# Kernel tuning notes

Hardware: AMD Instinct MI355X
Metric: run time of the kernel (lower is better)

Reference implementation:

```python
import jax, jax.numpy as jnp
from jax import lax
import numpy as np

H = 256        # hidden_dim
PRED_LEN = 96  # pred_len
B, L = 256, 512


def _gru_step(h, xt, W_ih, W_hh, b_ih, b_hh):
    # PyTorch GRU gate math. xt: [B, in], h: [B, H], W_ih: [3H, in], W_hh: [3H, H]
    gi = xt @ W_ih.T + b_ih            # [B, 3H]
    gh = h @ W_hh.T + b_hh             # [B, 3H]
    i_r, i_z, i_n = jnp.split(gi, 3, axis=-1)
    h_r, h_z, h_n = jnp.split(gh, 3, axis=-1)
    r = jax.nn.sigmoid(i_r + h_r)
    z = jax.nn.sigmoid(i_z + h_z)
    n = jnp.tanh(i_n + r * h_n)
    return (1.0 - z) * n + z * h


def _run_gru_layer(xs, W_ih, W_hh, b_ih, b_hh):
    # xs: [L, B, in] -> (ys [L, B, H], h_last [B, H])
    h0 = jnp.zeros((xs.shape[1], H), xs.dtype)
    def step(h, xt):
        hn = _gru_step(h, xt, W_ih, W_hh, b_ih, b_hh)
        return hn, hn
    h_last, ys = lax.scan(step, h0, xs)
    return ys, h_last


def setup_inputs() -> dict:
    key = jax.random.key(0)
    ks = jax.random.split(key, 16)
    s = 1.0 / np.sqrt(H)
    u = lambda k, shape: jax.random.uniform(k, shape, jnp.float32, -s, s)
    return {
        "x": jax.random.normal(ks[0], (B, 1, L), jnp.float32),
        # encoder GRU layer 0 (input_size=1)
        "W_ih0": u(ks[1], (3 * H, 1)), "W_hh0": u(ks[2], (3 * H, H)),
        "b_ih0": u(ks[3], (3 * H,)), "b_hh0": u(ks[4], (3 * H,)),
        # encoder GRU layer 1 (input_size=H)
        "W_ih1": u(ks[5], (3 * H, H)), "W_hh1": u(ks[6], (3 * H, H)),
        "b_ih1": u(ks[7], (3 * H,)), "b_hh1": u(ks[8], (3 * H,)),
        # decoder GRUCell (input_size=1)
        "Wd_ih": u(ks[9], (3 * H, 1)), "Wd_hh": u(ks[10], (3 * H, H)),
        "bd_ih": u(ks[11], (3 * H,)), "bd_hh": u(ks[12], (3 * H,)),
        # output Linear(H, 1)
        "Wo": u(ks[13], (1, H)), "bo": u(ks[14], (1,)),
    }


def reference(x, W_ih0, W_hh0, b_ih0, b_hh0, W_ih1, W_hh1, b_ih1, b_hh1,
              Wd_ih, Wd_hh, bd_ih, bd_hh, Wo, bo):
    # seq = x[:, 0, :].unsqueeze(-1) -> [B, L, 1]; scan wants [L, B, 1]
    xs = jnp.transpose(x[:, 0, :, None], (1, 0, 2))
    ys0, _ = _run_gru_layer(xs, W_ih0, W_hh0, b_ih0, b_hh0)
    _, h_t = _run_gru_layer(ys0, W_ih1, W_hh1, b_ih1, b_hh1)  # h_n[-1]: [B, H]
    # (dropout between layers is inactive in eval mode)

    dec_in0 = jnp.zeros((x.shape[0], 1), x.dtype)

    def dec_step(carry, _):
        h, inp = carry
        h = _gru_step(h, inp, Wd_ih, Wd_hh, bd_ih, bd_hh)
        step = h @ Wo.T + bo           # [B, 1]
        return (h, step), step

    _, steps = lax.scan(dec_step, (h_t, dec_in0), None, length=PRED_LEN)
    # steps: [pred_len, B, 1] -> cat along dim 1 -> [B, pred_len]
    return jnp.transpose(steps[..., 0], (1, 0))
```

## Files before the change

kernel.cpp:

```cpp
#include <hip/hip_runtime.h>
#include <hip/hip_fp16.h>

#define HDIM 256
#define LSEQ 512
#define PRED 96
#define NTHR 256

typedef _Float16 f16x8 __attribute__((ext_vector_type(8)));
typedef _Float16 f16x4 __attribute__((ext_vector_type(4)));
typedef float f32x4 __attribute__((ext_vector_type(4)));
typedef unsigned int u32;

__device__ __forceinline__ float sigm(float x) { return 1.f / (1.f + __expf(-x)); }
__device__ __forceinline__ float tanh_(float x) { float t = __expf(2.f * x); return 1.f - 2.f / (t + 1.f); }
__device__ __forceinline__ float dppx1(float v) {
  return __builtin_bit_cast(float, __builtin_amdgcn_update_dpp(
      0, __builtin_bit_cast(int, v), 0xB1, 0xF, 0xF, true));
}

struct __align__(16) Smem {
  _Float16 h[2][2][256];
  _Float16 A11[4][5120];
  float tw[3][256], tb[3][256], bnh[256], wo[256];
  float xv[LSEQ];
  float red[2][4];
};

#define CAST_A(DST, SRC) asm("" : "=a"(DST) : "0"(SRC))

#define DECL_MM                                                                \
  f16x8 Aa[6][8];                                                \
  f16x8 Av[5][8];                                                \
  f32x4 ac[12];                                      \
  f32x4 zc;                                          \
  { f32x4 z4 = {0.f, 0.f, 0.f, 0.f}; asm("" : "=a"(zc) : "0"(z4)); }

#define LOADA(WPTR)                                                            \
  _Pragma("unroll") for (int tt = 0; tt < 12; ++tt) {                          \
    _Pragma("unroll") for (int kt = 0; kt < 8; ++kt) {                         \
      const float* ap = (WPTR) +                                               \
          (size_t)(256 * (tt >> 2) + 64 * w + 16 * (tt & 3) + n) * HDIM +      \
          32 * kt + 8 * q;                                                     \
      const float4 a0 = *(const float4*)ap;                                    \
      const float4 a1 = *(const float4*)(ap + 4);                              \
      f16x8 tf;                                                                \
      tf[0] = (_Float16)a0.x; tf[1] = (_Float16)a0.y;                          \
      tf[2] = (_Float16)a0.z; tf[3] = (_Float16)a0.w;                          \
      tf[4] = (_Float16)a1.x; tf[5] = (_Float16)a1.y;                          \
      tf[6] = (_Float16)a1.z; tf[7] = (_Float16)a1.w;                          \
      if (tt < 6) { CAST_A(Aa[tt][kt], tf); }                                  \
      else if (tt < 11) { Av[tt - 6][kt] = tf; }                               \
      else { *(f16x8*)(a11p + kt * 1280) = tf; }                               \
    }                                                                          \
  }

#define MM_A_S(I, AF, B) asm("v_mfma_f32_16x16x32_f16 %0, %1, %2, %3" : "=a"(ac[I]) : "a"(AF), "v"(B), "a"(zc));
#define MM_A(I, AF, B)   asm("v_mfma_f32_16x16x32_f16 %0, %1, %2, %0" : "+a"(ac[I]) : "a"(AF), "v"(B));
#define MM_V_S(I, AF, B) asm("v_mfma_f32_16x16x32_f16 %0, %1, %2, %3" : "=a"(ac[I]) : "v"(AF), "v"(B), "a"(zc));
#define MM_V(I, AF, B)   asm("v_mfma_f32_16x16x32_f16 %0, %1, %2, %0" : "+a"(ac[I]) : "v"(AF), "v"(B));

#define R12S(KT, B, AL)                                                        \
  MM_A_S(0, Aa[0][KT], B) MM_A_S(1, Aa[1][KT], B) MM_A_S(2, Aa[2][KT], B)      \
  MM_A_S(3, Aa[3][KT], B) MM_A_S(4, Aa[4][KT], B) MM_A_S(5, Aa[5][KT], B)      \
  MM_V_S(6, Av[0][KT], B) MM_V_S(7, Av[1][KT], B) MM_V_S(8, Av[2][KT], B)      \
  MM_V_S(9, Av[3][KT], B) MM_V_S(10, Av[4][KT], B) MM_V_S(11, AL, B)
#define R12(KT, B, AL)                                                         \
  MM_A(0, Aa[0][KT], B) MM_A(1, Aa[1][KT], B) MM_A(2, Aa[2][KT], B)            \
  MM_A(3, Aa[3][KT], B) MM_A(4, Aa[4][KT], B) MM_A(5, Aa[5][KT], B)            \
  MM_V(6, Av[0][KT], B) MM_V(7, Av[1][KT], B) MM_V(8, Av[2][KT], B)            \
  MM_V(9, Av[3][KT], B) MM_V(10, Av[4][KT], B) MM_V(11, AL, B)

#define MAT_STEP(PB)                                                           \
  {                                                                            \
    const char* hp = hq + (PB) * 1024;                                         \
    f16x8 b0 = *(const f16x8*)(hp);                                            \
    f16x8 b1 = *(const f16x8*)(hp + 64);                                       \
    f16x8 b2 = *(const f16x8*)(hp + 128);                                      \
    f16x8 b3 = *(const f16x8*)(hp + 192);                                      \
    f16x8 a0 = *(const f16x8*)(a11p);                                          \
    f16x8 a1 = *(const f16x8*)(a11p + 1280);                                   \
    f16x8 a2 = *(const f16x8*)(a11p + 2560);                                   \
    f16x8 a3 = *(const f16x8*)(a11p + 3840);                                   \
    R12S(0, b0, a0)                                                            \
    b0 = *(const f16x8*)(hp + 256); a0 = *(const f16x8*)(a11p + 5120);         \
    R12(1, b1, a1)                                                             \
    b1 = *(const f16x8*)(hp + 320); a1 = *(const f16x8*)(a11p + 6400);         \
    R12(2, b2, a2)                                                             \
    b2 = *(const f16x8*)(hp + 384); a2 = *(const f16x8*)(a11p + 7680);         \
    R12(3, b3, a3)                                                             \
    b3 = *(const f16x8*)(hp + 448); a3 = *(const f16x8*)(a11p + 8960);         \
    R12(4, b0, a0)                                                             \
    R12(5, b1, a1)                                                             \
    R12(6, b2, a2)                                                             \
    R12(7, b3, a3)                                                             \
  }

#define ACFENCE                                                                \
  asm volatile("s_nop 7\n\ts_nop 7"                                            \
               : "+a"(ac[0]), "+a"(ac[1]), "+a"(ac[2]), "+a"(ac[3]),           \
                 "+a"(ac[4]), "+a"(ac[5]), "+a"(ac[6]), "+a"(ac[7]),           \
                 "+a"(ac[8]), "+a"(ac[9]), "+a"(ac[10]), "+a"(ac[11]));

#define BAR asm volatile("s_waitcnt lgkmcnt(0)\n\ts_barrier" ::: "memory")

#define SELG(P, G)                                                             \
  f32x4 P;                                                                     \
  { const f32x4 e0 = ac[4 * (G)], e1 = ac[4 * (G) + 1];                        \
    const f32x4 e2 = ac[4 * (G) + 2], e3 = ac[4 * (G) + 3];                    \
    const f32x4 t0 = s1 ? e1 : e0;                                             \
    const f32x4 t1 = s1 ? e3 : e2;                                             \
    P = s2 ? t1 : t0; }
#define PSUM(P)                                                                \
  { P[0] += dppx1(P[0]); P[1] += dppx1(P[1]);                                  \
    P[2] += dppx1(P[2]); P[3] += dppx1(P[3]); }

#define GATES(GR, GZ, GN, RHOOK, STEXTRA)                                      \
  {                                                                            \
    const char* rh = hrow + pb * 1024;                                         \
    char* wh = hrow + (pb ^ 1) * 1024;                                         \
    const f16x4 hh = *(const f16x4*)(rh);                                      \
    const f16x4 hl = *(const f16x4*)(rh + 512);                                \
    const f32x4 bn4 = *(const f32x4*)bnrow;                                    \
    f16x4 vh, vl;                                                              \
    _Pragma("unroll") for (int r = 0; r < 4; ++r) {                            \
      const float rr = sigm((GR)[r] + pr[r]);                                  \
      const float zz = sigm((GZ)[r] + pz[r]);                                  \
      const float nn = tanh_(fmaf(rr, pn[r] + bn4[r], (GN)[r]));               \
      const float ho = (float)hh[r] + (float)hl[r];                            \
      const float hv = fmaf(zz, ho - nn, nn);                                  \
      vh[r] = (_Float16)hv;                                                    \
      vl[r] = (_Float16)(hv - (float)vh[r]);                                   \
      RHOOK                                                                    \
    }                                                                          \
    if (st) {                                                                  \
      *(f16x4*)(wh) = vh;                                                      \
      *(f16x4*)(wh + 512) = vl;                                                \
      STEXTRA                                                                  \
    }                                                                          \
  }

#define LANE_GEOM                                                              \
  const int tid = threadIdx.x;                                                 \
  const int w = tid >> 6, lane = tid & 63, n = lane & 15, q = lane >> 4;       \
  const int b = blockIdx.x;                                                    \
  const int sg = (n >> 1) & 3;                                                 \
  const bool s1 = (n & 2) != 0, s2 = (n & 4) != 0;                             \
  const bool st = (n == 2 * sg);     \
  const int row = 64 * w + 16 * sg + 4 * q;                                    \
  char* a11p = (char*)sm.A11 + w * 10240 + n * 80 + q * 16;                    \
  const char* hq = (const char*)sm.h + (n & 1) * 512 + q * 16;                 \
  char* hrow = (char*)sm.h + row * 2;                                          \
  const char* bnrow = (const char*)sm.bnh + row * 4;

__global__ __launch_bounds__(NTHR, 1) void gru_l0(
    const float* __restrict__ x, const float* __restrict__ Wih0,
    const float* __restrict__ Whh0, const float* __restrict__ bih0,
    const float* __restrict__ bhh0, __half* __restrict__ ys) {
  __shared__ Smem sm;
  LANE_GEOM
  DECL_MM
  const float* twrow = (const float*)sm.tw + row;
  const float* tbrow = (const float*)sm.tb + row;

  for (int e = tid; e < LSEQ; e += NTHR) sm.xv[e] = x[(size_t)b * LSEQ + e];
#pragma unroll
  for (int g = 0; g < 3; ++g) {
    sm.tw[g][tid] = Wih0[256 * g + tid];
    sm.tb[g][tid] = bih0[256 * g + tid] + (g < 2 ? bhh0[256 * g + tid] : 0.f);
  }
  sm.bnh[tid] = bhh0[512 + tid];
  ((u32*)sm.h)[tid] = 0;
  LOADA(Whh0);
  __syncthreads();

  __half* ysp = ys + (size_t)b * LSEQ * HDIM + row;
  int pb = 0;
#pragma unroll 1
  for (int t = 0; t < LSEQ; ++t) {
    const float xt = sm.xv[t];
    MAT_STEP(pb)
    ACFENCE
    SELG(pr, 0) SELG(pz, 1) SELG(pn, 2)
    PSUM(pr) PSUM(pz) PSUM(pn)
    const f32x4 gr = *(const f32x4*)(twrow) * xt + *(const f32x4*)(tbrow);
    const f32x4 gz = *(const f32x4*)(twrow + 256) * xt + *(const f32x4*)(tbrow + 256);
    const f32x4 gn = *(const f32x4*)(twrow + 512) * xt + *(const f32x4*)(tbrow + 512);
    GATES(gr, gz, gn, ;, *(f16x4*)ysp = vh;)
    ysp += HDIM;
    pb ^= 1;
    BAR;
  }
}

__global__ __launch_bounds__(256) void gemm_gi(
    const float* __restrict__ Wih1, const float* __restrict__ bih1,
    const float* __restrict__ bhh1, const __half* __restrict__ ys,
    __half* __restrict__ gi) {
  const int lane = threadIdx.x & 63;
  const int wv = threadIdx.x >> 6;
  const size_t bt0 = (size_t)blockIdx.x << 4;
  const int n = lane & 15, q = lane >> 4;

  f16x8 bfr[8];
  const __half* yrow = ys + (bt0 + n) * HDIM + q * 8;
#pragma unroll
  for (int kk = 0; kk < 8; ++kk) bfr[kk] = *(const f16x8*)(yrow + kk * 32);

#pragma unroll 1
  for (int mt = 0; mt < 12; ++mt) {
    const int j0 = (wv * 12 + mt) << 4;
    const float* arow = Wih1 + (size_t)(j0 + n) * HDIM + q * 8;
    f32x4 acc = {0.f, 0.f, 0.f, 0.f};
#pragma unroll
    for (int kk = 0; kk < 8; ++kk) {
      const float4 a0 = *(const float4*)(arow + kk * 32);
      const float4 a1 = *(const float4*)(arow + kk * 32 + 4);
      f16x8 af;
      af[0] = (_Float16)a0.x; af[1] = (_Float16)a0.y;
      af[2] = (_Float16)a0.z; af[3] = (_Float16)a0.w;
      af[4] = (_Float16)a1.x; af[5] = (_Float16)a1.y;
      af[6] = (_Float16)a1.z; af[7] = (_Float16)a1.w;
      acc = __builtin_amdgcn_mfma_f32_16x16x32_f16(af, bfr[kk], acc, 0, 0, 0);
    }
    const int jr = j0 + (q << 2);
    __half o4[4];
#pragma unroll
    for (int r2 = 0; r2 < 4; ++r2) {
      const float bb = bih1[jr + r2] + (j0 < 512 ? bhh1[jr + r2] : 0.f);
      o4[r2] = __float2half(acc[r2] + bb);
    }
    *(uint2*)(gi + (bt0 + n) * 768 + jr) = *(uint2*)o4;
  }
}

#define LOADGI(PF, T)                                                          \
  { const __half* gp = gi + ((size_t)b * LSEQ + (T)) * 768 + row;              \
    PF[0] = *(const uint2*)(gp);                                               \
    PF[1] = *(const uint2*)(gp + 256);                                         \
    PF[2] = *(const uint2*)(gp + 512); }

#define STEP3(PF)                                                              \
  {                                                                            \
    MAT_STEP(pb)                                                               \
    ACFENCE                                                                    \
    SELG(pr, 0) SELG(pz, 1) SELG(pn, 2)                                        \
    PSUM(pr) PSUM(pz) PSUM(pn)                                                 \
    const __half2* p0 = (const __half2*)&PF[0];                                \
    const __half2* p1 = (const __half2*)&PF[1];                                \
    const __half2* p2 = (const __half2*)&PF[2];                                \
    const float2 r01 = __half22float2(p0[0]), r23 = __half22float2(p0[1]);     \
    const float2 z01 = __half22float2(p1[0]), z23 = __half22float2(p1[1]);     \
    const float2 n01 = __half22float2(p2[0]), n23 = __half22float2(p2[1]);     \
    const f32x4 gr = {r01.x, r01.y, r23.x, r23.y};                             \
    const f32x4 gz = {z01.x, z01.y, z23.x, z23.y};                             \
    const f32x4 gn = {n01.x, n01.y, n23.x, n23.y};                             \
    GATES(gr, gz, gn, ;, ;)                                                    \
    pb ^= 1;                                                                   \
    BAR;                                                                       \
  }

__global__ __launch_bounds__(NTHR, 1) void gru_l1dec(
    const float* __restrict__ Whh1, const float* __restrict__ bhh1,
    const float* __restrict__ Wdih, const float* __restrict__ Wdhh,
    const float* __restrict__ bdih, const float* __restrict__ bdhh,
    const float* __restrict__ Wo, const float* __restrict__ bo,
    const __half* __restrict__ gi, float* __restrict__ outp) {
  __shared__ Smem sm;
  LANE_GEOM
  DECL_MM
  const float* twrow = (const float*)sm.tw + row;
  const float* tbrow = (const float*)sm.tb + row;
  const float* worow = (const float*)sm.wo + row;

  sm.bnh[tid] = bhh1[512 + tid];
  ((u32*)sm.h)[tid] = 0;
  LOADA(Whh1);
  __syncthreads();

  uint2 pfA[3], pfB[3];
  LOADGI(pfA, 0);
  int pb = 0;
#pragma unroll 1
  for (int t = 0; t < LSEQ; t += 2) {
    LOADGI(pfB, t + 1);
    STEP3(pfA)
    LOADGI(pfA, (t + 2 < LSEQ) ? (t + 2) : (LSEQ - 1));
    STEP3(pfB)
  }

  LOADA(Wdhh);
#pragma unroll
  for (int g = 0; g < 3; ++g) {
    sm.tw[g][tid] = Wdih[256 * g + tid];
    sm.tb[g][tid] = bdih[256 * g + tid] + (g < 2 ? bdhh[256 * g + tid] : 0.f);
  }
  sm.bnh[tid] = bdhh[512 + tid];
  sm.wo[tid] = Wo[tid];
  const float bov = bo[0];
  if (tid < 4) sm.red[0][tid] = (tid == 0) ? -bov : 0.f;
  __syncthreads();

  int rb = 0;
#pragma unroll 1
  for (int t = 0; t < PRED; ++t) {
    const f32x4 rd = *(const f32x4*)sm.red[rb];
    const float it = bov + rd[0] + rd[1] + rd[2] + rd[3];
    if (tid == 0 && t > 0) outp[(size_t)b * PRED + t - 1] = it;
    MAT_STEP(pb)
    ACFENCE
    SELG(pr, 0) SELG(pz, 1) SELG(pn, 2)
    PSUM(pr) PSUM(pz) PSUM(pn)
    const f32x4 gr = *(const f32x4*)(twrow) * it + *(const f32x4*)(tbrow);
    const f32x4 gz = *(const f32x4*)(twrow + 256) * it + *(const f32x4*)(tbrow + 256);
    const f32x4 gn = *(const f32x4*)(twrow + 512) * it + *(const f32x4*)(tbrow + 512);
    const f32x4 wo4 = *(const f32x4*)worow;
    float c = 0.f;
    GATES(gr, gz, gn, c = fmaf(wo4[r], hv, c);, ;)
    if (!st) c = 0.f;
    c += __shfl_xor(c, 2);
    c += __shfl_xor(c, 4);
    c += __shfl_xor(c, 16);
    c += __shfl_xor(c, 32);
    if (lane == 0) sm.red[rb ^ 1][w] = c;
    pb ^= 1;
    rb ^= 1;
    BAR;
  }
  if (tid == 0) {
    const f32x4 rd = *(const f32x4*)sm.red[rb];
    outp[(size_t)b * PRED + PRED - 1] = bov + rd[0] + rd[1] + rd[2] + rd[3];
  }
}

extern "C" void kernel_launch(void* const* d_in, const int* in_sizes, int n_in,
                              void* d_out, int out_size, void* d_ws, size_t ws_size,
                              hipStream_t stream) {
  const float* x    = (const float*)d_in[0];
  const float* Wih0 = (const float*)d_in[1];
  const float* Whh0 = (const float*)d_in[2];
  const float* bih0 = (const float*)d_in[3];
  const float* bhh0 = (const float*)d_in[4];
  const float* Wih1 = (const float*)d_in[5];
  const float* Whh1 = (const float*)d_in[6];
  const float* bih1 = (const float*)d_in[7];
  const float* bhh1 = (const float*)d_in[8];
  const float* Wdih = (const float*)d_in[9];
  const float* Wdhh = (const float*)d_in[10];
  const float* bdih = (const float*)d_in[11];
  const float* bdhh = (const float*)d_in[12];
  const float* Wo   = (const float*)d_in[13];
  const float* bo   = (const float*)d_in[14];

  __half* ys = (__half*)d_ws;
  __half* gi = ys + (size_t)256 * 512 * 256;

  gru_l0<<<256, NTHR, 0, stream>>>(x, Wih0, Whh0, bih0, bhh0, ys);
  gemm_gi<<<(256 * 512) / 16, 256, 0, stream>>>(Wih1, bih1, bhh1, ys, gi);
  gru_l1dec<<<256, NTHR, 0, stream>>>(Whh1, bhh1, Wdih, Wdhh, bdih, bdhh,
                                      Wo, bo, gi, (float*)d_out);
}
```

Baseline: 2.651 ms.

## Stream pre-packed fp16 recurrent weights from global with 8 waves per block

Adds a prep kernel that converts the three recurrent weight matrices to fp16 once and stores them in an MFMA-fragment-friendly layout in a global buffer. The recurrent kernels now use 512 threads (8 waves) and reload half of the weight fragments from global/L2 every timestep while issuing MFMAs, instead of keeping all weights in registers plus LDS. This frees register and LDS pressure and spreads the per-step matmul across twice as many waves, at the cost of per-step global weight traffic and an extra launch.

```diff
diff --git a/kernel.cpp b/kernel.cpp
--- a/kernel.cpp
+++ b/kernel.cpp
@@ -4,12 +4,14 @@
 #define HDIM 256
 #define LSEQ 512
 #define PRED 96
-#define NTHR 256
+#define NTHR 512
 
 typedef _Float16 f16x8 __attribute__((ext_vector_type(8)));
 typedef _Float16 f16x4 __attribute__((ext_vector_type(4)));
 typedef float f32x4 __attribute__((ext_vector_type(4)));
 typedef unsigned int u32;
+
+__device__ __align__(16) _Float16 wpk_g[3 * 196608];
 
 __device__ __forceinline__ float sigm(float x) { return 1.f / (1.f + __expf(-x)); }
 __device__ __forceinline__ float tanh_(float x) { float t = __expf(2.f * x); return 1.f - 2.f / (t + 1.f); }
@@ -20,105 +22,72 @@
 
 struct __align__(16) Smem {
   _Float16 h[2][2][256];
-  _Float16 A11[4][5120];
   float tw[3][256], tb[3][256], bnh[256], wo[256];
   float xv[LSEQ];
-  float red[2][4];
+  float red[2][8];
 };
 
-#define CAST_A(DST, SRC) asm("" : "=a"(DST) : "0"(SRC))
-
-#define DECL_MM                                                                \
-  f16x8 Aa[6][8];                                                \
-  f16x8 Av[5][8];                                                \
-  f32x4 ac[12];                                      \
-  f32x4 zc;                                          \
-  { f32x4 z4 = {0.f, 0.f, 0.f, 0.f}; asm("" : "=a"(zc) : "0"(z4)); }
-
-#define LOADA(WPTR)                                                            \
-  _Pragma("unroll") for (int tt = 0; tt < 12; ++tt) {                          \
-    _Pragma("unroll") for (int kt = 0; kt < 8; ++kt) {                         \
-      const float* ap = (WPTR) +                                               \
-          (size_t)(256 * (tt >> 2) + 64 * w + 16 * (tt & 3) + n) * HDIM +      \
-          32 * kt + 8 * q;                                                     \
-      const float4 a0 = *(const float4*)ap;                                    \
-      const float4 a1 = *(const float4*)(ap + 4);                              \
-      f16x8 tf;                                                                \
-      tf[0] = (_Float16)a0.x; tf[1] = (_Float16)a0.y;                          \
-      tf[2] = (_Float16)a0.z; tf[3] = (_Float16)a0.w;                          \
-      tf[4] = (_Float16)a1.x; tf[5] = (_Float16)a1.y;                          \
-      tf[6] = (_Float16)a1.z; tf[7] = (_Float16)a1.w;                          \
-      if (tt < 6) { CAST_A(Aa[tt][kt], tf); }                                  \
-      else if (tt < 11) { Av[tt - 6][kt] = tf; }                               \
-      else { *(f16x8*)(a11p + kt * 1280) = tf; }                               \
-    }                                                                          \
-  }
-
-#define MM_A_S(I, AF, B) asm("v_mfma_f32_16x16x32_f16 %0, %1, %2, %3" : "=a"(ac[I]) : "a"(AF), "v"(B), "a"(zc));
-#define MM_A(I, AF, B)   asm("v_mfma_f32_16x16x32_f16 %0, %1, %2, %0" : "+a"(ac[I]) : "a"(AF), "v"(B));
-#define MM_V_S(I, AF, B) asm("v_mfma_f32_16x16x32_f16 %0, %1, %2, %3" : "=a"(ac[I]) : "v"(AF), "v"(B), "a"(zc));
-#define MM_V(I, AF, B)   asm("v_mfma_f32_16x16x32_f16 %0, %1, %2, %0" : "+a"(ac[I]) : "v"(AF), "v"(B));
-
-#define R12S(KT, B, AL)                                                        \
-  MM_A_S(0, Aa[0][KT], B) MM_A_S(1, Aa[1][KT], B) MM_A_S(2, Aa[2][KT], B)      \
-  MM_A_S(3, Aa[3][KT], B) MM_A_S(4, Aa[4][KT], B) MM_A_S(5, Aa[5][KT], B)      \
-  MM_V_S(6, Av[0][KT], B) MM_V_S(7, Av[1][KT], B) MM_V_S(8, Av[2][KT], B)      \
-  MM_V_S(9, Av[3][KT], B) MM_V_S(10, Av[4][KT], B) MM_V_S(11, AL, B)
-#define R12(KT, B, AL)                                                         \
-  MM_A(0, Aa[0][KT], B) MM_A(1, Aa[1][KT], B) MM_A(2, Aa[2][KT], B)            \
-  MM_A(3, Aa[3][KT], B) MM_A(4, Aa[4][KT], B) MM_A(5, Aa[5][KT], B)            \
-  MM_V(6, Av[0][KT], B) MM_V(7, Av[1][KT], B) MM_V(8, Av[2][KT], B)            \
-  MM_V(9, Av[3][KT], B) MM_V(10, Av[4][KT], B) MM_V(11, AL, B)
-
-#define MAT_STEP(PB)                                                           \
-  {                                                                            \
-    const char* hp = hq + (PB) * 1024;                                         \
-    f16x8 b0 = *(const f16x8*)(hp);                                            \
-    f16x8 b1 = *(const f16x8*)(hp + 64);                                       \
-    f16x8 b2 = *(const f16x8*)(hp + 128);                                      \
-    f16x8 b3 = *(const f16x8*)(hp + 192);                                      \
-    f16x8 a0 = *(const f16x8*)(a11p);                                          \
-    f16x8 a1 = *(const f16x8*)(a11p + 1280);                                   \
-    f16x8 a2 = *(const f16x8*)(a11p + 2560);                                   \
-    f16x8 a3 = *(const f16x8*)(a11p + 3840);                                   \
-    R12S(0, b0, a0)                                                            \
-    b0 = *(const f16x8*)(hp + 256); a0 = *(const f16x8*)(a11p + 5120);         \
-    R12(1, b1, a1)                                                             \
-    b1 = *(const f16x8*)(hp + 320); a1 = *(const f16x8*)(a11p + 6400);         \
-    R12(2, b2, a2)                                                             \
-    b2 = *(const f16x8*)(hp + 384); a2 = *(const f16x8*)(a11p + 7680);         \
-    R12(3, b3, a3)                                                             \
-    b3 = *(const f16x8*)(hp + 448); a3 = *(const f16x8*)(a11p + 8960);         \
-    R12(4, b0, a0)                                                             \
-    R12(5, b1, a1)                                                             \
-    R12(6, b2, a2)                                                             \
-    R12(7, b3, a3)                                                             \
-  }
-
-#define ACFENCE                                                                \
-  asm volatile("s_nop 7\n\ts_nop 7"                                            \
-               : "+a"(ac[0]), "+a"(ac[1]), "+a"(ac[2]), "+a"(ac[3]),           \
-                 "+a"(ac[4]), "+a"(ac[5]), "+a"(ac[6]), "+a"(ac[7]),           \
-                 "+a"(ac[8]), "+a"(ac[9]), "+a"(ac[10]), "+a"(ac[11]));
-
-#define BAR asm volatile("s_waitcnt lgkmcnt(0)\n\ts_barrier" ::: "memory")
-
-#define SELG(P, G)                                                             \
-  f32x4 P;                                                                     \
-  { const f32x4 e0 = ac[4 * (G)], e1 = ac[4 * (G) + 1];                        \
-    const f32x4 e2 = ac[4 * (G) + 2], e3 = ac[4 * (G) + 3];                    \
-    const f32x4 t0 = s1 ? e1 : e0;                                             \
-    const f32x4 t1 = s1 ? e3 : e2;                                             \
-    P = s2 ? t1 : t0; }
+#define DECL8                                                                  \
+  f32x4 ac[6];                 \
+  f32x4 zc;                                                                    \
+  { f32x4 z4 = {0.f, 0.f, 0.f, 0.f}; asm("" : "=a"(zc) : "0"(z4)); }           \
+  f16x8 wA[6], wB[6], wC[6], wD[6];
+
+#define LOADW(DST, KT)                                                         \
+  { _Pragma("unroll") for (int tau = 0; tau < 6; ++tau)                        \
+      DST[tau] = *(const f16x8*)(wbase + ((KT) * 6 + tau) * 512 + lane * 8); }
+
+#define MMW_S(I, AF, B) asm volatile("v_mfma_f32_16x16x32_f16 %0, %1, %2, %3" : "=a"(ac[I]) : "v"(AF), "v"(B), "a"(zc));
+#define MMW(I, AF, B)   asm volatile("v_mfma_f32_16x16x32_f16 %0, %1, %2, %0" : "+a"(ac[I]) : "v"(AF), "v"(B));
+#define MM6_S(WF, B) MMW_S(0, WF[0], B) MMW_S(1, WF[1], B) MMW_S(2, WF[2], B)  \
+                     MMW_S(3, WF[3], B) MMW_S(4, WF[4], B) MMW_S(5, WF[5], B)
+#define MM6(WF, B)   MMW(0, WF[0], B) MMW(1, WF[1], B) MMW(2, WF[2], B)        \
+                     MMW(3, WF[3], B) MMW(4, WF[4], B) MMW(5, WF[5], B)
+
+#define VMW0 asm volatile("s_waitcnt vmcnt(0)" ::: "memory");
+
+#define FENCE                                                                  \
+  asm volatile("s_nop 7\n\ts_nop 7\n\ts_nop 7\n\ts_nop 7\n\t"                  \
+               "s_nop 7\n\ts_nop 7\n\ts_nop 7\n\ts_nop 7"                      \
+               : "+a"(ac[0]), "+a"(ac[1]), "+a"(ac[2]),                        \
+                 "+a"(ac[3]), "+a"(ac[4]), "+a"(ac[5]));                       \
+  __builtin_amdgcn_sched_barrier(0);
+
+#define BAR asm volatile("s_waitcnt vmcnt(0) lgkmcnt(0)\n\ts_barrier" ::: "memory")
+
+#define SELG2(P, G)                                                            \
+  { const f32x4 e0 = ac[2 * (G)], e1 = ac[2 * (G) + 1]; P = s1 ? e1 : e0; }
 #define PSUM(P)                                                                \
   { P[0] += dppx1(P[0]); P[1] += dppx1(P[1]);                                  \
     P[2] += dppx1(P[2]); P[3] += dppx1(P[3]); }
 
-#define GATES(GR, GZ, GN, RHOOK, STEXTRA)                                      \
+#define LDH(OFF) (*(const f16x8*)(hp + (OFF)))
+
+#define MCORE8(PB, ...)                                                        \
+  {                                                                            \
+    const char* hp = hq + (PB) * 1024;                                         \
+    f16x8 u0 = LDH(0), u1 = LDH(64), u2 = LDH(128), u3 = LDH(192);             \
+    __VA_ARGS__                                                                \
+    MM6_S(wA, u0) u0 = LDH(256); LOADW(wA, 4)                                  \
+    MM6(wB, u1)   u1 = LDH(320); LOADW(wB, 5)                                  \
+    MM6(wC, u2)   u2 = LDH(384); LOADW(wC, 6)                                  \
+    MM6(wD, u3)   u3 = LDH(448); LOADW(wD, 7)                                  \
+    VMW0                                                                       \
+    MM6(wA, u0)   LOADW(wA, 0)                                                 \
+    MM6(wB, u1)   LOADW(wB, 1)                                                 \
+    MM6(wC, u2)   LOADW(wC, 2)                                                 \
+    MM6(wD, u3)   LOADW(wD, 3)                                                 \
+    FENCE                                                                      \
+    SELG2(pr, 0) PSUM(pr)                                                      \
+    SELG2(pz, 1) PSUM(pz)                                                      \
+    SELG2(pn, 2) PSUM(pn)                                                      \
+  }
+
+#define GTAIL8(GR, GZ, GN, RHOOK, STEXTRA)                                     \
   {                                                                            \
     const char* rh = hrow + pb * 1024;                                         \
     char* wh = hrow + (pb ^ 1) * 1024;                                         \
-    const f16x4 hh = *(const f16x4*)(rh);                                      \
+    const f16x4 hh = *(const f16x4*)rh;                                        \
     const f16x4 hl = *(const f16x4*)(rh + 512);                                \
     const f32x4 bn4 = *(const f32x4*)bnrow;                                    \
     f16x4 vh, vl;                                                              \
@@ -133,44 +102,71 @@
       RHOOK                                                                    \
     }                                                                          \
     if (st) {                                                                  \
-      *(f16x4*)(wh) = vh;                                                      \
+      *(f16x4*)wh = vh;                                                        \
       *(f16x4*)(wh + 512) = vl;                                                \
       STEXTRA                                                                  \
     }                                                                          \
   }
 
-#define LANE_GEOM                                                              \
+#define LANE_GEOM8                                                             \
   const int tid = threadIdx.x;                                                 \
   const int w = tid >> 6, lane = tid & 63, n = lane & 15, q = lane >> 4;       \
   const int b = blockIdx.x;                                                    \
-  const int sg = (n >> 1) & 3;                                                 \
-  const bool s1 = (n & 2) != 0, s2 = (n & 4) != 0;                             \
-  const bool st = (n == 2 * sg);     \
-  const int row = 64 * w + 16 * sg + 4 * q;                                    \
-  char* a11p = (char*)sm.A11 + w * 10240 + n * 80 + q * 16;                    \
+  const bool s1 = (n & 2) != 0;                                                \
+  const bool st = (n & 13) == 0;      \
+  const int sg1 = (n >> 1) & 1;                                                \
+  const int row = 32 * w + 16 * sg1 + 4 * q;                                   \
   const char* hq = (const char*)sm.h + (n & 1) * 512 + q * 16;                 \
   char* hrow = (char*)sm.h + row * 2;                                          \
   const char* bnrow = (const char*)sm.bnh + row * 4;
 
-__global__ __launch_bounds__(NTHR, 1) void gru_l0(
-    const float* __restrict__ x, const float* __restrict__ Wih0,
-    const float* __restrict__ Whh0, const float* __restrict__ bih0,
-    const float* __restrict__ bhh0, __half* __restrict__ ys) {
+__global__ __launch_bounds__(256) void prep(const float* __restrict__ W0,
+                                            const float* __restrict__ W1,
+                                            const float* __restrict__ Wd) {
+  const int idx = blockIdx.x * 256 + threadIdx.x;
+  const int lane = idx & 63;
+  int t2 = idx >> 6;
+  const int tau = t2 % 6; t2 /= 6;
+  const int kt = t2 & 7;  t2 >>= 3;
+  const int w = t2 & 7;   t2 >>= 3;
+  const int L = t2;
+  const float* W = (L == 0) ? W0 : ((L == 1) ? W1 : Wd);
+  const int g = tau >> 1, s = tau & 1, n = lane & 15, q = lane >> 4;
+  const int r = 256 * g + 32 * w + 16 * s + n;
+  const int c = 32 * kt + 8 * q;
+  const float4 a0 = *(const float4*)(W + (size_t)r * HDIM + c);
+  const float4 a1 = *(const float4*)(W + (size_t)r * HDIM + c + 4);
+  f16x8 tf;
+  tf[0] = (_Float16)a0.x; tf[1] = (_Float16)a0.y;
+  tf[2] = (_Float16)a0.z; tf[3] = (_Float16)a0.w;
+  tf[4] = (_Float16)a1.x; tf[5] = (_Float16)a1.y;
+  tf[6] = (_Float16)a1.z; tf[7] = (_Float16)a1.w;
+  *(f16x8*)(wpk_g + (size_t)L * 196608 + (size_t)w * 24576 +
+            (kt * 6 + tau) * 512 + lane * 8) = tf;
+}
+
+__global__ __attribute__((amdgpu_flat_work_group_size(NTHR, NTHR), amdgpu_waves_per_eu(2)))
+void gru_l0(const float* __restrict__ x, const float* __restrict__ Wih0,
+            const float* __restrict__ bih0, const float* __restrict__ bhh0,
+            __half* __restrict__ ys) {
   __shared__ Smem sm;
-  LANE_GEOM
-  DECL_MM
-  const float* twrow = (const float*)sm.tw + row;
-  const float* tbrow = (const float*)sm.tb + row;
-
-  for (int e = tid; e < LSEQ; e += NTHR) sm.xv[e] = x[(size_t)b * LSEQ + e];
-#pragma unroll
-  for (int g = 0; g < 3; ++g) {
-    sm.tw[g][tid] = Wih0[256 * g + tid];
-    sm.tb[g][tid] = bih0[256 * g + tid] + (g < 2 ? bhh0[256 * g + tid] : 0.f);
-  }
-  sm.bnh[tid] = bhh0[512 + tid];
+  LANE_GEOM8
+  DECL8
+  const _Float16* wbase = wpk_g + (size_t)w * 24576;
+  const char* twp = (const char*)sm.tw + row * 4;
+  const char* tbp = (const char*)sm.tb + row * 4;
+
+  sm.xv[tid] = x[(size_t)b * LSEQ + tid];
+  if (tid < 256) {
+#pragma unroll
+    for (int g = 0; g < 3; ++g) {
+      sm.tw[g][tid] = Wih0[256 * g + tid];
+      sm.tb[g][tid] = bih0[256 * g + tid] + (g < 2 ? bhh0[256 * g + tid] : 0.f);
+    }
+    sm.bnh[tid] = bhh0[512 + tid];
+  }
   ((u32*)sm.h)[tid] = 0;
-  LOADA(Whh0);
+  LOADW(wA, 0) LOADW(wB, 1) LOADW(wC, 2) LOADW(wD, 3)
   __syncthreads();
 
   __half* ysp = ys + (size_t)b * LSEQ * HDIM + row;
@@ -178,14 +174,12 @@
 #pragma unroll 1
   for (int t = 0; t < LSEQ; ++t) {
     const float xt = sm.xv[t];
-    MAT_STEP(pb)
-    ACFENCE
-    SELG(pr, 0) SELG(pz, 1) SELG(pn, 2)
-    PSUM(pr) PSUM(pz) PSUM(pn)
-    const f32x4 gr = *(const f32x4*)(twrow) * xt + *(const f32x4*)(tbrow);
-    const f32x4 gz = *(const f32x4*)(twrow + 256) * xt + *(const f32x4*)(tbrow + 256);
-    const f32x4 gn = *(const f32x4*)(twrow + 512) * xt + *(const f32x4*)(tbrow + 512);
-    GATES(gr, gz, gn, ;, *(f16x4*)ysp = vh;)
+    f32x4 pr, pz, pn;
+    MCORE8(pb, ;)
+    const f32x4 g_r = *(const f32x4*)twp * xt + *(const f32x4*)tbp;
+    const f32x4 g_z = *(const f32x4*)(twp + 1024) * xt + *(const f32x4*)(tbp + 1024);
+    const f32x4 g_n = *(const f32x4*)(twp + 2048) * xt + *(const f32x4*)(tbp + 2048);
+    GTAIL8(g_r, g_z, g_n, ;, *(f16x4*)ysp = vh;)
     ysp += HDIM;
     pb ^= 1;
     BAR;
@@ -239,86 +233,77 @@
     PF[1] = *(const uint2*)(gp + 256);                                         \
     PF[2] = *(const uint2*)(gp + 512); }
 
-#define STEP3(PF)                                                              \
-  {                                                                            \
-    MAT_STEP(pb)                                                               \
-    ACFENCE                                                                    \
-    SELG(pr, 0) SELG(pz, 1) SELG(pn, 2)                                        \
-    PSUM(pr) PSUM(pz) PSUM(pn)                                                 \
-    const __half2* p0 = (const __half2*)&PF[0];                                \
-    const __half2* p1 = (const __half2*)&PF[1];                                \
-    const __half2* p2 = (const __half2*)&PF[2];                                \
-    const float2 r01 = __half22float2(p0[0]), r23 = __half22float2(p0[1]);     \
-    const float2 z01 = __half22float2(p1[0]), z23 = __half22float2(p1[1]);     \
-    const float2 n01 = __half22float2(p2[0]), n23 = __half22float2(p2[1]);     \
-    const f32x4 gr = {r01.x, r01.y, r23.x, r23.y};                             \
-    const f32x4 gz = {z01.x, z01.y, z23.x, z23.y};                             \
-    const f32x4 gn = {n01.x, n01.y, n23.x, n23.y};                             \
-    GATES(gr, gz, gn, ;, ;)                                                    \
-    pb ^= 1;                                                                   \
-    BAR;                                                                       \
-  }
-
-__global__ __launch_bounds__(NTHR, 1) void gru_l1dec(
-    const float* __restrict__ Whh1, const float* __restrict__ bhh1,
-    const float* __restrict__ Wdih, const float* __restrict__ Wdhh,
-    const float* __restrict__ bdih, const float* __restrict__ bdhh,
-    const float* __restrict__ Wo, const float* __restrict__ bo,
-    const __half* __restrict__ gi, float* __restrict__ outp) {
+__global__ __attribute__((amdgpu_flat_work_group_size(NTHR, NTHR), amdgpu_waves_per_eu(2)))
+void gru_l1dec(const float* __restrict__ bhh1, const float* __restrict__ Wdih,
+               const float* __restrict__ bdih, const float* __restrict__ bdhh,
+               const float* __restrict__ Wo, const float* __restrict__ bo,
+               const __half* __restrict__ gi, float* __restrict__ outp) {
   __shared__ Smem sm;
-  LANE_GEOM
-  DECL_MM
-  const float* twrow = (const float*)sm.tw + row;
-  const float* tbrow = (const float*)sm.tb + row;
-  const float* worow = (const float*)sm.wo + row;
-
-  sm.bnh[tid] = bhh1[512 + tid];
+  LANE_GEOM8
+  DECL8
+  const _Float16* wbase = wpk_g + 196608 + (size_t)w * 24576;
+  const char* twp = (const char*)sm.tw + row * 4;
+  const char* tbp = (const char*)sm.tb + row * 4;
+  const char* wop = (const char*)sm.wo + row * 4;
+
+  if (tid < 256) sm.bnh[tid] = bhh1[512 + tid];
   ((u32*)sm.h)[tid] = 0;
-  LOADA(Whh1);
+  LOADW(wA, 0) LOADW(wB, 1) LOADW(wC, 2) LOADW(wD, 3)
   __syncthreads();
 
-  uint2 pfA[3], pfB[3];
-  LOADGI(pfA, 0);
   int pb = 0;
 #pragma unroll 1
-  for (int t = 0; t < LSEQ; t += 2) {
-    LOADGI(pfB, t + 1);
-    STEP3(pfA)
-    LOADGI(pfA, (t + 2 < LSEQ) ? (t + 2) : (LSEQ - 1));
-    STEP3(pfB)
-  }
-
-  LOADA(Wdhh);
-#pragma unroll
-  for (int g = 0; g < 3; ++g) {
-    sm.tw[g][tid] = Wdih[256 * g + tid];
-    sm.tb[g][tid] = bdih[256 * g + tid] + (g < 2 ? bdhh[256 * g + tid] : 0.f);
-  }
-  sm.bnh[tid] = bdhh[512 + tid];
-  sm.wo[tid] = Wo[tid];
+  for (int t = 0; t < LSEQ; ++t) {
+    uint2 pf[3];
+    f32x4 pr, pz, pn;
+    MCORE8(pb, LOADGI(pf, t))
+    const __half2* p0 = (const __half2*)&pf[0];
+    const __half2* p1 = (const __half2*)&pf[1];
+    const __half2* p2 = (const __half2*)&pf[2];
+    const float2 r01 = __half22float2(p0[0]), r23 = __half22float2(p0[1]);
+    const float2 z01 = __half22float2(p1[0]), z23 = __half22float2(p1[1]);
+    const float2 n01 = __half22float2(p2[0]), n23 = __half22float2(p2[1]);
+    const f32x4 g_r = {r01.x, r01.y, r23.x, r23.y};
+    const f32x4 g_z = {z01.x, z01.y, z23.x, z23.y};
+    const f32x4 g_n = {n01.x, n01.y, n23.x, n23.y};
+    GTAIL8(g_r, g_z, g_n, ;, ;)
+    pb ^= 1;
+    BAR;
+  }
+
+  wbase = wpk_g + 2 * 196608 + (size_t)w * 24576;
+  if (tid < 256) {
+#pragma unroll
+    for (int g = 0; g < 3; ++g) {
+      sm.tw[g][tid] = Wdih[256 * g + tid];
+      sm.tb[g][tid] = bdih[256 * g + tid] + (g < 2 ? bdhh[256 * g + tid] : 0.f);
+    }
+    sm.bnh[tid] = bdhh[512 + tid];
+    sm.wo[tid] = Wo[tid];
+  }
   const float bov = bo[0];
-  if (tid < 4) sm.red[0][tid] = (tid == 0) ? -bov : 0.f;
+  if (tid < 8) sm.red[0][tid] = (tid == 0) ? -bov : 0.f;
+  LOADW(wA, 0) LOADW(wB, 1) LOADW(wC, 2) LOADW(wD, 3)
   __syncthreads();
 
   int rb = 0;
 #pragma unroll 1
   for (int t = 0; t < PRED; ++t) {
-    const f32x4 rd = *(const f32x4*)sm.red[rb];
-    const float it = bov + rd[0] + rd[1] + rd[2] + rd[3];
+    const f32x4 rd0 = *(const f32x4*)sm.red[rb];
+    const f32x4 rd1 = *(const f32x4*)(&sm.red[rb][4]);
+    const float it = bov + rd0[0] + rd0[1] + rd0[2] + rd0[3] +
+                     rd1[0] + rd1[1] + rd1[2] + rd1[3];
     if (tid == 0 && t > 0) outp[(size_t)b * PRED + t - 1] = it;
-    MAT_STEP(pb)
-    ACFENCE
-    SELG(pr, 0) SELG(pz, 1) SELG(pn, 2)
-    PSUM(pr) PSUM(pz) PSUM(pn)
-    const f32x4 gr = *(const f32x4*)(twrow) * it + *(const f32x4*)(tbrow);
-    const f32x4 gz = *(const f32x4*)(twrow + 256) * it + *(const f32x4*)(tbrow + 256);
-    const f32x4 gn = *(const f32x4*)(twrow + 512) * it + *(const f32x4*)(tbrow + 512);
-    const f32x4 wo4 = *(const f32x4*)worow;
+    f32x4 pr, pz, pn;
+    MCORE8(pb, ;)
+    const f32x4 g_r = *(const f32x4*)twp * it + *(const f32x4*)tbp;
+    const f32x4 g_z = *(const f32x4*)(twp + 1024) * it + *(const f32x4*)(tbp + 1024);
+    const f32x4 g_n = *(const f32x4*)(twp + 2048) * it + *(const f32x4*)(tbp + 2048);
+    const f32x4 wo4 = *(const f32x4*)wop;
     float c = 0.f;
-    GATES(gr, gz, gn, c = fmaf(wo4[r], hv, c);, ;)
+    GTAIL8(g_r, g_z, g_n, c = fmaf(wo4[r], hv, c);, ;)
     if (!st) c = 0.f;
     c += __shfl_xor(c, 2);
-    c += __shfl_xor(c, 4);
     c += __shfl_xor(c, 16);
     c += __shfl_xor(c, 32);
     if (lane == 0) sm.red[rb ^ 1][w] = c;
@@ -327,8 +312,10 @@
     BAR;
   }
   if (tid == 0) {
-    const f32x4 rd = *(const f32x4*)sm.red[rb];
-    outp[(size_t)b * PRED + PRED - 1] = bov + rd[0] + rd[1] + rd[2] + rd[3];
+    float ov = bov;
+#pragma unroll
+    for (int ww = 0; ww < 8; ++ww) ov += sm.red[rb][ww];
+    outp[(size_t)b * PRED + PRED - 1] = ov;
   }
 }
 
@@ -354,8 +341,9 @@
   __half* ys = (__half*)d_ws;
   __half* gi = ys + (size_t)256 * 512 * 256;
 
-  gru_l0<<<256, NTHR, 0, stream>>>(x, Wih0, Whh0, bih0, bhh0, ys);
+  prep<<<288, 256, 0, stream>>>(Whh0, Whh1, Wdhh);
+  gru_l0<<<256, NTHR, 0, stream>>>(x, Wih0, bih0, bhh0, ys);
   gemm_gi<<<(256 * 512) / 16, 256, 0, stream>>>(Wih1, bih1, bhh1, ys, gi);
-  gru_l1dec<<<256, NTHR, 0, stream>>>(Whh1, bhh1, Wdih, Wdhh, bdih, bdhh,
-                                      Wo, bo, gi, (float*)d_out);
-}
+  gru_l1dec<<<256, NTHR, 0, stream>>>(bhh1, Wdih, bdih, bdhh, Wo, bo,
+                                      gi, (float*)d_out);
+}
```

Measured after the change: 5.120 ms. 93.2% more time.
